# Kernel optimization log

Hardware: AMD Instinct MI355X
Metric: run time of the kernel (lower is better)

## Reference

```python
import jax, jax.numpy as jnp
import numpy as np

B, T, CIN, HID, OUT, H, W = 8, 8, 128, 64, 64, 32, 32


def _conv(x, w, b):
    # x: [B, C, H, W], w: [O, C, kh, kw] -> SAME-padded conv, stride 1
    y = jax.lax.conv_general_dilated(x, w, (1, 1), "SAME",
                                     dimension_numbers=("NCHW", "OIHW", "NCHW"))
    return y + b[None, :, None, None]


def _layer_dir(xs, w_ih, w_hh, b_ih, b_hh, reverse):
    # xs: [T, B, C, H, W]; one direction of a ConvLSTM layer; returns hs [T, B, HID, H, W]
    b, hh_, ww_ = xs.shape[1], xs.shape[3], xs.shape[4]
    h0 = jnp.zeros((b, HID, hh_, ww_), xs.dtype)

    def step(carry, x):
        h, c = carry
        gates = _conv(x, w_ih, b_ih) + _conv(h, w_hh, b_hh)  # [B, 4*HID, H, W]
        i, f, g, o = jnp.split(gates, 4, axis=1)
        c = jax.nn.sigmoid(f) * c + jax.nn.sigmoid(i) * jnp.tanh(g)
        h = jax.nn.sigmoid(o) * jnp.tanh(c)
        return (h, c), h

    _, hs = jax.lax.scan(step, (h0, h0), xs, reverse=reverse)
    return hs


def _forward(features, w_ih0f, w_hh0f, b_ih0f, b_hh0f,
             w_ih0r, w_hh0r, b_ih0r, b_hh0r,
             w_ih1f, w_hh1f, b_ih1f, b_hh1f,
             w_ih1r, w_hh1r, b_ih1r, b_hh1r,
             w_out, b_out):
    xs = jnp.transpose(features, (1, 0, 2, 3, 4))  # [T, B, C, H, W]
    # layer 0, both directions (scan reverse=True aligns outputs to original time order)
    hf = _layer_dir(xs, w_ih0f, w_hh0f, b_ih0f, b_hh0f, False)
    hr = _layer_dir(xs, w_ih0r, w_hh0r, b_ih0r, b_hh0r, True)
    xs1 = jnp.concatenate([hf, hr], axis=2)  # [T, B, 2*HID, H, W] (dropout is identity at eval)
    # layer 1
    hf1 = _layer_dir(xs1, w_ih1f, w_hh1f, b_ih1f, b_hh1f, False)
    hr1 = _layer_dir(xs1, w_ih1r, w_hh1r, b_ih1r, b_hh1r, True)
    last = jnp.concatenate([hf1[-1], hr1[-1]], axis=1)  # output[:, -1] -> [B, 2*HID, H, W]
    return jax.nn.relu(_conv(last, w_out, b_out))


def setup_inputs() -> dict:
    key = jax.random.key(0)
    ks = jax.random.split(key, 24)
    G = 4 * HID
    p = lambda k, s: jax.random.normal(k, s, jnp.float32) * 0.05
    d = {"features": jax.random.normal(ks[0], (B, T, CIN, H, W), jnp.float32)}
    i = 1
    for l, cin in ((0, CIN), (1, 2 * HID)):
        for dr in ("f", "r"):
            d[f"w_ih{l}{dr}"] = p(ks[i], (G, cin, 3, 3)); i += 1
            d[f"w_hh{l}{dr}"] = p(ks[i], (G, HID, 3, 3)); i += 1
            d[f"b_ih{l}{dr}"] = p(ks[i], (G,)); i += 1
            d[f"b_hh{l}{dr}"] = p(ks[i], (G,)); i += 1
    d["w_out"] = p(ks[i], (OUT, 2 * HID, 1, 1)); i += 1
    d["b_out"] = p(ks[i], (OUT,))
    return d


def reference(features, w_ih0f, w_hh0f, b_ih0f, b_hh0f,
              w_ih0r, w_hh0r, b_ih0r, b_hh0r,
              w_ih1f, w_hh1f, b_ih1f, b_hh1f,
              w_ih1r, w_hh1r, b_ih1r, b_hh1r,
              w_out, b_out):
    return _forward(features, w_ih0f, w_hh0f, b_ih0f, b_hh0f,
                    w_ih0r, w_hh0r, b_ih0r, b_hh0r,
                    w_ih1f, w_hh1f, b_ih1f, b_hh1f,
                    w_ih1r, w_hh1r, b_ih1r, b_hh1r,
                    w_out, b_out)
```

## Files before the change

kernel.cpp:

```cpp
#include <hip/hip_runtime.h>
#include <math.h>
#include <stdint.h>


typedef __attribute__((ext_vector_type(8))) short short8;
typedef __attribute__((ext_vector_type(4))) float float4v;

namespace {
constexpr int IMG = 34 * 34 * 64;
constexpr size_t SLOTI = 16ull * IMG;
constexpr int ROWB = 34 * 128;
constexpr int PADB = 8192;
}
template <int N> struct IC { static constexpr int v = N; };

__device__ __forceinline__ uint16_t bf16_rne(float x) {
  uint32_t u = __builtin_bit_cast(uint32_t, x);
  return (uint16_t)((u + 0x7FFFu + ((u >> 16) & 1u)) >> 16);
}
__device__ __forceinline__ float bf16_to_f(uint16_t h) {
  uint32_t u = ((uint32_t)h) << 16;
  return __builtin_bit_cast(float, u);
}

__device__ __forceinline__ void gl_lds16(const void* g, void* l) {
  __builtin_amdgcn_global_load_lds(
      (const __attribute__((address_space(1))) void*)g,
      (__attribute__((address_space(3))) void*)l, 16, 0, 0);
}

__global__ void pack_features(const float* __restrict__ f, uint16_t* __restrict__ out) {
  const size_t i = (size_t)blockIdx.x * 256 + threadIdx.x;
  const int blk_s = (int)(i & 7);
  size_t pp = i >> 3;
  const int px = (int)(pp % 34); pp /= 34;
  const int yy = (int)(pp % 34); pp /= 34;
  const int cg = (int)(pp & 3);
  const int bt = (int)(pp >> 2);
  const int b = bt & 7, t = bt >> 3;
  const int blk = blk_s ^ (px & 7);
  const int pl = blk >> 2, kg = blk & 3;
  short8 sv;
  if (px == 0 || px == 33 || yy == 0 || yy == 33) {
    #pragma unroll
    for (int j = 0; j < 8; ++j) sv[j] = 0;
  } else {
    const int x = px - 1, y = yy - 1;
    #pragma unroll
    for (int j = 0; j < 8; ++j) {
      const int ch = cg * 32 + kg * 8 + j;
      const float fv = f[(((size_t)b * 8 + t) * 128 + ch) * 1024 + y * 32 + x];
      const uint16_t hi = bf16_rne(fv);
      sv[j] = (short)(pl ? bf16_rne(fv - bf16_to_f(hi)) : hi);
    }
  }
  *(short8*)(out + i * 8) = sv;
}

struct WPackArgs {
  const float* wih[4]; const float* whh[4];
  const float* bih[4]; const float* bhh[4];
  uint32_t* wp; float* bp;
};
__global__ void pack_weights(WPackArgs A) {
  const int combo = blockIdx.y;
  const int idx = blockIdx.x * 256 + threadIdx.x;
  const int q = idx & 4095;
  const int rest = idx >> 12;
  const int nt = rest & 1;
  const int ct = rest >> 1;
  const int tap = ct % 9, cg = ct / 9;
  const int w2 = q & 3;
  const int b8s = (q >> 2) & 7;
  const int hcp = (q >> 5) & 15;
  const int g = (q >> 9) & 3;
  const int pl = (q >> 11) & 1;
  const int b8 = b8s ^ (hcp & 7);
  const int kg = b8 & 3;
  const int hcl = hcp * 2 + (b8 >> 2);
  const int n = g * 64 + nt * 32 + hcl;
  const float* wih = A.wih[combo];
  const float* whh = A.whh[combo];
  uint32_t out = 0;
  #pragma unroll
  for (int e = 0; e < 2; ++e) {
    const int ch = cg * 32 + kg * 8 + w2 * 2 + e;
    const float wv = (ch < 128) ? wih[((size_t)n * 128 + ch) * 9 + tap]
                                : whh[((size_t)n * 64 + (ch - 128)) * 9 + tap];
    const uint16_t hi = bf16_rne(wv);
    const uint16_t v = pl ? bf16_rne(wv - bf16_to_f(hi)) : hi;
    out |= ((uint32_t)v) << (16 * e);
  }
  A.wp[(size_t)combo * 442368 + idx] = out;
  if (idx < 256) A.bp[combo * 256 + idx] = A.bih[combo][idx] + A.bhh[combo][idx];
}

struct StepArgs {
  const uint16_t* in0; const uint16_t* in1; const uint16_t* in2;
  int nc0, nc1, nc2;
  const uint32_t* W;
  const float* bias;
  float* cbuf;
  uint16_t* himg;
  float* hf32;
};

template <int ROWS>
__global__ __launch_bounds__(ROWS * 128, ROWS / 2) void conv_lstm_step(StepArgs A0, StepArgs A1) {
  constexpr int NW = ROWS * 2;
  constexpr int THREADS = NW * 64;
  constexpr int BANDS = 32 / ROWS;
  constexpr int LOGB = (ROWS == 4) ? 3 : 4;
  constexpr int ACH = (ROWS == 4) ? 4 : 5;
  constexpr int ASLOT = ACH * NW * 1024;
  constexpr int WCH = 16384 / (NW * 1024);
  constexpr int CNT0 = WCH;
  constexpr int CNT12 = WCH + ACH;

  extern __shared__ char smem[];
  char* Asm_ = smem;
  char* Wsm_ = smem + 2 * ASLOT;

  const StepArgs a = (blockIdx.z == 0) ? A0 : A1;
  const int bx = blockIdx.x;
  const int nt = bx & 1;
  const int band = (bx >> 1) & (BANDS - 1);
  const int b = bx >> (1 + LOGB);
  const int y0 = band * ROWS;
  const int tid = threadIdx.x;
  const int lane = tid & 63;
  const int w = tid >> 6;
  const int m15 = lane & 15;
  const int kg = lane >> 4;
  const int r = w & (ROWS - 1);
  const int hcg = (ROWS == 4) ? (w >> 2) : (w >> 1);

  int offA[2][3][2];
  #pragma unroll
  for (int xh = 0; xh < 2; ++xh)
    #pragma unroll
    for (int kx = 0; kx < 3; ++kx)
      #pragma unroll
      for (int pl = 0; pl < 2; ++pl) {
        const int px = xh * 16 + kx + m15;
        const int sw = (pl * 4 + kg) ^ (px & 7);
        offA[xh][kx][pl] = r * ROWB + px * 128 + sw * 16;
      }
  int offW[2][4];
  {
    const int hcp = hcg * 8 + (m15 >> 1);
    const int b8 = kg + 4 * (m15 & 1);
    #pragma unroll
    for (int pl = 0; pl < 2; ++pl)
      #pragma unroll
      for (int g = 0; g < 4; ++g)
        offW[pl][g] = (((pl * 4 + g) * 16 + hcp) * 8 + (b8 ^ (hcp & 7))) * 16;
  }

  const int ncg = a.nc0 + a.nc1 + a.nc2;
  auto abase = [&](int cg) -> const char* {
    const uint16_t* t;
    if (cg < a.nc0) t = a.in0 + ((size_t)b * a.nc0 + cg) * IMG;
    else if (cg < a.nc0 + a.nc1) t = a.in1 + ((size_t)b * a.nc1 + (cg - a.nc0)) * IMG;
    else t = a.in2 + ((size_t)b * a.nc2 + (cg - a.nc0 - a.nc1)) * IMG;
    return (const char*)t + (size_t)y0 * ROWB;
  };
  auto stageA = [&](int cgi, int par) {
    const char* g = abase(cgi);
    char* d = Asm_ + par * ASLOT;
    #pragma unroll
    for (int j = 0; j < ACH; ++j)
      gl_lds16(g + (size_t)(ACH * w + j) * 1024 + lane * 16, d + (ACH * w + j) * 1024);
  };
  auto stageW = [&](int cgs, int taps, int slot) {
    const char* g = (const char*)a.W + ((size_t)((cgs * 9 + taps) * 2 + nt) << 14);
    char* d = Wsm_ + slot * 16384;
    #pragma unroll
    for (int j = 0; j < WCH; ++j)
      gl_lds16(g + (size_t)(WCH * w + j) * 1024 + lane * 16, d + (WCH * w + j) * 1024);
  };

  float4v acc[2][4];
  #pragma unroll
  for (int xh = 0; xh < 2; ++xh)
    #pragma unroll
    for (int g = 0; g < 4; ++g) acc[xh][g] = (float4v){0.f, 0.f, 0.f, 0.f};

  stageA(0, 0);
  stageW(0, 0, 0);
  stageW(0, 1, 1);

  for (int cg = 0; cg < ncg; ++cg) {
    auto tap_body = [&](auto tapc) {
      constexpr int TAP = decltype(tapc)::v;
      constexpr int CNT = (TAP == 1 || TAP == 2) ? CNT12 : CNT0;
      asm volatile("s_waitcnt vmcnt(%0)\n\ts_barrier" :: "n"(CNT) : "memory");
      const int lin = cg * 9 + TAP;
      {
        const int l2 = lin + 2;
        int cgs = l2 / 9;
        const int taps = l2 % 9;
        if (cgs >= ncg) cgs = 0;
        stageW(cgs, taps, l2 % 3);
      }
      if (TAP == 0) {
        const int nx = (cg + 1 < ncg) ? cg + 1 : 0;
        stageA(nx, (cg + 1) & 1);
      }
      constexpr int ky = TAP / 3, kx = TAP % 3;
      const char* Ab = Asm_ + (cg & 1) * ASLOT + ky * ROWB;
      const char* Wb = Wsm_ + (lin % 3) * 16384;
      short8 af[2][2];
      #pragma unroll
      for (int xh = 0; xh < 2; ++xh)
        #pragma unroll
        for (int pl = 0; pl < 2; ++pl)
          af[xh][pl] = *(const short8*)(Ab + offA[xh][kx][pl]);
      short8 wfr[2][4];
      #pragma unroll
      for (int pl = 0; pl < 2; ++pl)
        #pragma unroll
        for (int g = 0; g < 4; ++g)
          wfr[pl][g] = *(const short8*)(Wb + offW[pl][g]);
      #pragma unroll
      for (int xh = 0; xh < 2; ++xh)
        #pragma unroll
        for (int g = 0; g < 4; ++g) {
          acc[xh][g] = __builtin_amdgcn_mfma_f32_16x16x32_bf16(af[xh][0], wfr[0][g], acc[xh][g], 0, 0, 0);
          acc[xh][g] = __builtin_amdgcn_mfma_f32_16x16x32_bf16(af[xh][0], wfr[1][g], acc[xh][g], 0, 0, 0);
          acc[xh][g] = __builtin_amdgcn_mfma_f32_16x16x32_bf16(af[xh][1], wfr[0][g], acc[xh][g], 0, 0, 0);
        }
    };
    tap_body(IC<0>{}); tap_body(IC<1>{}); tap_body(IC<2>{});
    tap_body(IC<3>{}); tap_body(IC<4>{}); tap_body(IC<5>{});
    tap_body(IC<6>{}); tap_body(IC<7>{}); tap_body(IC<8>{});
  }
  asm volatile("s_waitcnt vmcnt(0)" ::: "memory");

  const int hcl = hcg * 16 + m15;
  const int hc = nt * 32 + hcl;
  const int y = y0 + r;
  float bi[4];
  #pragma unroll
  for (int g = 0; g < 4; ++g) bi[g] = a.bias[g * 64 + hc];
  float* crow = a.cbuf + ((size_t)(b * 64 + hc)) * 1024 + y * 32;
  float* hrow = a.hf32 ? a.hf32 + ((size_t)(b * 64 + hc)) * 1024 + y * 32 : nullptr;
  uint16_t* hb = a.himg ? a.himg + ((size_t)(b * 2 + nt)) * IMG : nullptr;
  const int kgb = hcl >> 3, jj = hcl & 7;
  #pragma unroll
  for (int xh = 0; xh < 2; ++xh) {
    const int x0 = xh * 16 + kg * 4;
    float4v cv = *(float4v*)(crow + x0);
    float4v cn, hn;
    #pragma unroll
    for (int q = 0; q < 4; ++q) {
      const float ig = 1.f / (1.f + expf(-(acc[xh][0][q] + bi[0])));
      const float fg = 1.f / (1.f + expf(-(acc[xh][1][q] + bi[1])));
      const float gg = tanhf(acc[xh][2][q] + bi[2]);
      const float og = 1.f / (1.f + expf(-(acc[xh][3][q] + bi[3])));
      const float c2 = fg * cv[q] + ig * gg;
      cn[q] = c2;
      hn[q] = og * tanhf(c2);
    }
    *(float4v*)(crow + x0) = cn;
    if (hrow) *(float4v*)(hrow + x0) = hn;
    if (hb) {
      #pragma unroll
      for (int q = 0; q < 4; ++q) {
        const int px = x0 + q + 1;
        const int sw = px & 7;
        const uint16_t hi = bf16_rne(hn[q]);
        const uint16_t lo = bf16_rne(hn[q] - bf16_to_f(hi));
        const size_t p16 = ((size_t)(y + 1) * 34 + px) * 64;
        hb[p16 + (size_t)(kgb ^ sw) * 8 + jj] = hi;
        hb[p16 + (size_t)((4 + kgb) ^ sw) * 8 + jj] = lo;
      }
    }
  }
  if (hb) {
    {
      const int rr = tid >> 7;
      const int hlf = (tid >> 6) & 1;
      const int jx = tid & 63;
      hb[((size_t)(y0 + 1 + rr) * 34 + hlf * 33) * 64 + jx] = 0;
    }
    if (band == 0) for (int i = tid; i < 2176; i += THREADS) hb[i] = 0;
    if (band == BANDS - 1) for (int i = tid; i < 2176; i += THREADS) hb[(size_t)33 * 2176 + i] = 0;
  }
}

__global__ void final_conv(const float* __restrict__ h1f_last, const float* __restrict__ h1r_last,
                           const float* __restrict__ wout, const float* __restrict__ bout,
                           float* __restrict__ out) {
  __shared__ float Ws[16 * 128];
  const int oq = blockIdx.y;
  for (int i = threadIdx.x; i < 16 * 128; i += 256) Ws[i] = wout[oq * 16 * 128 + i];
  __syncthreads();
  const int gp = blockIdx.x * 256 + threadIdx.x;
  const int b = gp >> 10, p = gp & 1023;
  float acc[16];
  #pragma unroll
  for (int o = 0; o < 16; ++o) acc[o] = bout[oq * 16 + o];
  for (int c = 0; c < 128; ++c) {
    const float xv = (c < 64) ? h1f_last[((size_t)b * 64 + c) * 1024 + p]
                              : h1r_last[((size_t)b * 64 + (c - 64)) * 1024 + p];
    #pragma unroll
    for (int o = 0; o < 16; ++o) acc[o] = fmaf(xv, Ws[o * 128 + c], acc[o]);
  }
  #pragma unroll
  for (int o = 0; o < 16; ++o) {
    const float v = acc[o];
    out[((size_t)b * 64 + oq * 16 + o) * 1024 + p] = v > 0.f ? v : 0.f;
  }
}

extern "C" void kernel_launch(void* const* d_in, const int* in_sizes, int n_in,
                              void* d_out, int out_size, void* d_ws, size_t ws_size,
                              hipStream_t stream) {
  char* p = (char*)d_ws;
  uint16_t* featImg = (uint16_t*)p; p += (size_t)8 * 8 * 4 * IMG * 2 + PADB;
  uint32_t* WP = (uint32_t*)p;      p += (size_t)4 * 442368 * 4;
  float* bp = (float*)p;            p += 4096;
  uint16_t* hf0i = (uint16_t*)p;    p += (size_t)9 * SLOTI * 2 + PADB;
  uint16_t* hr0i = (uint16_t*)p;    p += (size_t)9 * SLOTI * 2 + PADB;
  uint16_t* h1fi = (uint16_t*)p;    p += (size_t)2 * SLOTI * 2 + PADB;
  float* c0f = (float*)p;           p += (size_t)4 * 2097152;
  float* c0r = c0f + 524288;
  float* c1f = c0r + 524288;
  float* c1r = c1f + 524288;
  float* h1f8 = (float*)p;          p += 2097152;
  float* h1r8 = (float*)p;          p += 2097152;

  hipMemsetAsync(c0f, 0, (size_t)4 * 2097152, stream);
  hipMemsetAsync(hf0i, 0, (size_t)SLOTI * 2, stream);
  hipMemsetAsync(hr0i + (size_t)8 * SLOTI, 0, (size_t)SLOTI * 2, stream);
  hipMemsetAsync(h1fi, 0, (size_t)SLOTI * 2, stream);

  pack_features<<<dim3(9248), 256, 0, stream>>>((const float*)d_in[0], featImg);

  WPackArgs wa;
  for (int combo = 0; combo < 4; ++combo) {
    const int base = 1 + combo * 4;
    wa.wih[combo] = (const float*)d_in[base];
    wa.whh[combo] = (const float*)d_in[base + 1];
    wa.bih[combo] = (const float*)d_in[base + 2];
    wa.bhh[combo] = (const float*)d_in[base + 3];
  }
  wa.wp = WP; wa.bp = bp;
  pack_weights<<<dim3(1728, 4), 256, 0, stream>>>(wa);

  constexpr int DYN4 = 2 * 32768 + 3 * 16384;
  constexpr int DYN2 = 2 * 20480 + 3 * 16384;
  (void)hipFuncSetAttribute((const void*)(conv_lstm_step<4>),
                            hipFuncAttributeMaxDynamicSharedMemorySize, DYN4);
  (void)hipFuncSetAttribute((const void*)(conv_lstm_step<2>),
                            hipFuncAttributeMaxDynamicSharedMemorySize, DYN2);

  auto mk = [&](const uint16_t* i0, int n0, const uint16_t* i1, int n1,
                const uint16_t* i2, int n2, int combo, float* cb,
                uint16_t* himg, float* hf32) {
    StepArgs s;
    s.in0 = i0; s.in1 = i1; s.in2 = i2;
    s.nc0 = n0; s.nc1 = n1; s.nc2 = n2;
    s.W = WP + (size_t)combo * 442368; s.bias = bp + combo * 256;
    s.cbuf = cb; s.himg = himg; s.hf32 = hf32;
    return s;
  };

  for (int k = 0; k < 8; ++k) {
    const int tr = 7 - k;
    StepArgs f = mk(featImg + (size_t)k * 8 * 4 * IMG, 4,
                    hf0i + (size_t)k * SLOTI, 2, nullptr, 0,
                    0, c0f, hf0i + (size_t)(k + 1) * SLOTI, nullptr);
    StepArgs r = mk(featImg + (size_t)tr * 8 * 4 * IMG, 4,
                    hr0i + (size_t)(tr + 1) * SLOTI, 2, nullptr, 0,
                    1, c0r, hr0i + (size_t)tr * SLOTI, nullptr);
    conv_lstm_step<4><<<dim3(128, 1, 2), 512, DYN4, stream>>>(f, r);
  }

  for (int t = 0; t < 8; ++t) {
    uint16_t* himg = (t < 7) ? h1fi + (size_t)((t + 1) & 1) * SLOTI : nullptr;
    float* hf32 = (t == 7) ? h1f8 : nullptr;
    StepArgs s = mk(hf0i + (size_t)(t + 1) * SLOTI, 2, hr0i + (size_t)t * SLOTI, 2,
                    h1fi + (size_t)(t & 1) * SLOTI, 2, 2, c1f, himg, hf32);
    if (t == 0) {
      StepArgs rv = mk(hf0i + (size_t)8 * SLOTI, 2, hr0i + (size_t)7 * SLOTI, 2,
                       nullptr, 0, 3, c1r, nullptr, h1r8);
      conv_lstm_step<4><<<dim3(128, 1, 2), 512, DYN4, stream>>>(s, rv);
    } else {
      conv_lstm_step<2><<<dim3(256, 1, 1), 256, DYN2, stream>>>(s, s);
    }
  }

  final_conv<<<dim3(32, 4), 256, 0, stream>>>(
      h1f8, h1r8, (const float*)d_in[17], (const float*)d_in[18], (float*)d_out);
}
```

Before: 725.5 us.

## Retile ConvLSTM step blocks to 16 channels and two rows per wave

Each block now covers 16 hidden channels (a quarter of the gate outputs) across more image rows, and every wave computes two output rows, so each weight fragment loaded from LDS feeds twice as many MFMAs. Weight staging per block is halved to 8KB per tap, while the input halo tile grows. Blocks have fewer waves (4 or 2) and launch bounds are relaxed to 1, which doubles accumulator registers per wave and lowers the wave count per block, so latency hiding may suffer.

```diff
diff --git a/kernel.cpp b/kernel.cpp
--- a/kernel.cpp
+++ b/kernel.cpp
@@ -105,15 +105,15 @@
   float* hf32;
 };
 
-template <int ROWS>
-__global__ __launch_bounds__(ROWS * 128, ROWS / 2) void conv_lstm_step(StepArgs A0, StepArgs A1) {
-  constexpr int NW = ROWS * 2;
+template <int ROWS, int NW>
+__global__ __launch_bounds__(NW * 64, 1) void conv_lstm_step(StepArgs A0, StepArgs A1) {
   constexpr int THREADS = NW * 64;
   constexpr int BANDS = 32 / ROWS;
-  constexpr int LOGB = (ROWS == 4) ? 3 : 4;
-  constexpr int ACH = (ROWS == 4) ? 4 : 5;
+  constexpr int BSH = (ROWS == 8) ? 2 : 3;
+  constexpr int ABYTES = (ROWS + 2) * ROWB;
+  constexpr int ACH = (ABYTES + NW * 1024 - 1) / (NW * 1024);
   constexpr int ASLOT = ACH * NW * 1024;
-  constexpr int WCH = 16384 / (NW * 1024);
+  constexpr int WCH = 8 / NW;
   constexpr int CNT0 = WCH;
   constexpr int CNT12 = WCH + ACH;
 
@@ -123,38 +123,40 @@
 
   const StepArgs a = (blockIdx.z == 0) ? A0 : A1;
   const int bx = blockIdx.x;
-  const int nt = bx & 1;
-  const int band = (bx >> 1) & (BANDS - 1);
-  const int b = bx >> (1 + LOGB);
+  const int Q4 = bx & 3;
+  const int band = (bx >> 2) & (BANDS - 1);
+  const int b = bx >> (2 + BSH);
+  const int nt = Q4 >> 1;
+  const int nq = Q4 & 1;
   const int y0 = band * ROWS;
   const int tid = threadIdx.x;
   const int lane = tid & 63;
   const int w = tid >> 6;
   const int m15 = lane & 15;
   const int kg = lane >> 4;
-  const int r = w & (ROWS - 1);
-  const int hcg = (ROWS == 4) ? (w >> 2) : (w >> 1);
-
-  int offA[2][3][2];
-  #pragma unroll
-  for (int xh = 0; xh < 2; ++xh)
-    #pragma unroll
-    for (int kx = 0; kx < 3; ++kx)
-      #pragma unroll
-      for (int pl = 0; pl < 2; ++pl) {
-        const int px = xh * 16 + kx + m15;
-        const int sw = (pl * 4 + kg) ^ (px & 7);
-        offA[xh][kx][pl] = r * ROWB + px * 128 + sw * 16;
-      }
+
+  int offA[2][2][3][2];
+  #pragma unroll
+  for (int row = 0; row < 2; ++row)
+    #pragma unroll
+    for (int xh = 0; xh < 2; ++xh)
+      #pragma unroll
+      for (int kx = 0; kx < 3; ++kx)
+        #pragma unroll
+        for (int pl = 0; pl < 2; ++pl) {
+          const int px = xh * 16 + kx + m15;
+          const int sw = (pl * 4 + kg) ^ (px & 7);
+          offA[row][xh][kx][pl] = (2 * w + row) * ROWB + px * 128 + sw * 16;
+        }
   int offW[2][4];
   {
-    const int hcp = hcg * 8 + (m15 >> 1);
+    const int hcpl = m15 >> 1;
     const int b8 = kg + 4 * (m15 & 1);
     #pragma unroll
     for (int pl = 0; pl < 2; ++pl)
       #pragma unroll
       for (int g = 0; g < 4; ++g)
-        offW[pl][g] = (((pl * 4 + g) * 16 + hcp) * 8 + (b8 ^ (hcp & 7))) * 16;
+        offW[pl][g] = (((pl * 4 + g) * 8 + hcpl) * 8 + (b8 ^ hcpl)) * 16;
   }
 
   const int ncg = a.nc0 + a.nc1 + a.nc2;
@@ -173,18 +175,23 @@
       gl_lds16(g + (size_t)(ACH * w + j) * 1024 + lane * 16, d + (ACH * w + j) * 1024);
   };
   auto stageW = [&](int cgs, int taps, int slot) {
-    const char* g = (const char*)a.W + ((size_t)((cgs * 9 + taps) * 2 + nt) << 14);
-    char* d = Wsm_ + slot * 16384;
-    #pragma unroll
-    for (int j = 0; j < WCH; ++j)
-      gl_lds16(g + (size_t)(WCH * w + j) * 1024 + lane * 16, d + (WCH * w + j) * 1024);
+    const char* g = (const char*)a.W + ((size_t)((cgs * 9 + taps) * 2 + nt) << 14)
+                  + (size_t)nq * 1024;
+    char* d = Wsm_ + slot * 8192;
+    #pragma unroll
+    for (int j = 0; j < WCH; ++j) {
+      const int c = WCH * w + j;
+      gl_lds16(g + (size_t)c * 2048 + lane * 16, d + c * 1024);
+    }
   };
 
-  float4v acc[2][4];
-  #pragma unroll
-  for (int xh = 0; xh < 2; ++xh)
-    #pragma unroll
-    for (int g = 0; g < 4; ++g) acc[xh][g] = (float4v){0.f, 0.f, 0.f, 0.f};
+  float4v acc[2][2][4];
+  #pragma unroll
+  for (int row = 0; row < 2; ++row)
+    #pragma unroll
+    for (int xh = 0; xh < 2; ++xh)
+      #pragma unroll
+      for (int g = 0; g < 4; ++g) acc[row][xh][g] = (float4v){0.f, 0.f, 0.f, 0.f};
 
   stageA(0, 0);
   stageW(0, 0, 0);
@@ -209,13 +216,15 @@
       }
       constexpr int ky = TAP / 3, kx = TAP % 3;
       const char* Ab = Asm_ + (cg & 1) * ASLOT + ky * ROWB;
-      const char* Wb = Wsm_ + (lin % 3) * 16384;
-      short8 af[2][2];
-      #pragma unroll
-      for (int xh = 0; xh < 2; ++xh)
+      const char* Wb = Wsm_ + (lin % 3) * 8192;
+      short8 af[2][2][2];
+      #pragma unroll
+      for (int row = 0; row < 2; ++row)
         #pragma unroll
-        for (int pl = 0; pl < 2; ++pl)
-          af[xh][pl] = *(const short8*)(Ab + offA[xh][kx][pl]);
+        for (int xh = 0; xh < 2; ++xh)
+          #pragma unroll
+          for (int pl = 0; pl < 2; ++pl)
+            af[row][xh][pl] = *(const short8*)(Ab + offA[row][xh][kx][pl]);
       short8 wfr[2][4];
       #pragma unroll
       for (int pl = 0; pl < 2; ++pl)
@@ -223,13 +232,15 @@
         for (int g = 0; g < 4; ++g)
           wfr[pl][g] = *(const short8*)(Wb + offW[pl][g]);
       #pragma unroll
-      for (int xh = 0; xh < 2; ++xh)
+      for (int row = 0; row < 2; ++row)
         #pragma unroll
-        for (int g = 0; g < 4; ++g) {
-          acc[xh][g] = __builtin_amdgcn_mfma_f32_16x16x32_bf16(af[xh][0], wfr[0][g], acc[xh][g], 0, 0, 0);
-          acc[xh][g] = __builtin_amdgcn_mfma_f32_16x16x32_bf16(af[xh][0], wfr[1][g], acc[xh][g], 0, 0, 0);
-          acc[xh][g] = __builtin_amdgcn_mfma_f32_16x16x32_bf16(af[xh][1], wfr[0][g], acc[xh][g], 0, 0, 0);
-        }
+        for (int xh = 0; xh < 2; ++xh)
+          #pragma unroll
+          for (int g = 0; g < 4; ++g) {
+            acc[row][xh][g] = __builtin_amdgcn_mfma_f32_16x16x32_bf16(af[row][xh][0], wfr[0][g], acc[row][xh][g], 0, 0, 0);
+            acc[row][xh][g] = __builtin_amdgcn_mfma_f32_16x16x32_bf16(af[row][xh][0], wfr[1][g], acc[row][xh][g], 0, 0, 0);
+            acc[row][xh][g] = __builtin_amdgcn_mfma_f32_16x16x32_bf16(af[row][xh][1], wfr[0][g], acc[row][xh][g], 0, 0, 0);
+          }
     };
     tap_body(IC<0>{}); tap_body(IC<1>{}); tap_body(IC<2>{});
     tap_body(IC<3>{}); tap_body(IC<4>{}); tap_body(IC<5>{});
@@ -237,51 +248,55 @@
   }
   asm volatile("s_waitcnt vmcnt(0)" ::: "memory");
 
-  const int hcl = hcg * 16 + m15;
-  const int hc = nt * 32 + hcl;
-  const int y = y0 + r;
+  const int hc = Q4 * 16 + m15;
   float bi[4];
   #pragma unroll
   for (int g = 0; g < 4; ++g) bi[g] = a.bias[g * 64 + hc];
-  float* crow = a.cbuf + ((size_t)(b * 64 + hc)) * 1024 + y * 32;
-  float* hrow = a.hf32 ? a.hf32 + ((size_t)(b * 64 + hc)) * 1024 + y * 32 : nullptr;
-  uint16_t* hb = a.himg ? a.himg + ((size_t)(b * 2 + nt)) * IMG : nullptr;
-  const int kgb = hcl >> 3, jj = hcl & 7;
-  #pragma unroll
-  for (int xh = 0; xh < 2; ++xh) {
-    const int x0 = xh * 16 + kg * 4;
-    float4v cv = *(float4v*)(crow + x0);
-    float4v cn, hn;
-    #pragma unroll
-    for (int q = 0; q < 4; ++q) {
-      const float ig = 1.f / (1.f + expf(-(acc[xh][0][q] + bi[0])));
-      const float fg = 1.f / (1.f + expf(-(acc[xh][1][q] + bi[1])));
-      const float gg = tanhf(acc[xh][2][q] + bi[2]);
-      const float og = 1.f / (1.f + expf(-(acc[xh][3][q] + bi[3])));
-      const float c2 = fg * cv[q] + ig * gg;
-      cn[q] = c2;
-      hn[q] = og * tanhf(c2);
-    }
-    *(float4v*)(crow + x0) = cn;
-    if (hrow) *(float4v*)(hrow + x0) = hn;
-    if (hb) {
+  const int img = Q4 >> 1;
+  const int chi = (Q4 & 1) * 16 + m15;
+  const int kgb = chi >> 3, jj = chi & 7;
+  uint16_t* hb = a.himg ? a.himg + ((size_t)(b * 2 + img)) * IMG : nullptr;
+  #pragma unroll
+  for (int row = 0; row < 2; ++row) {
+    const int y = y0 + 2 * w + row;
+    float* crow = a.cbuf + ((size_t)(b * 64 + hc)) * 1024 + y * 32;
+    float* hrow = a.hf32 ? a.hf32 + ((size_t)(b * 64 + hc)) * 1024 + y * 32 : nullptr;
+    #pragma unroll
+    for (int xh = 0; xh < 2; ++xh) {
+      const int x0 = xh * 16 + kg * 4;
+      float4v cv = *(float4v*)(crow + x0);
+      float4v cn, hn;
       #pragma unroll
       for (int q = 0; q < 4; ++q) {
-        const int px = x0 + q + 1;
-        const int sw = px & 7;
-        const uint16_t hi = bf16_rne(hn[q]);
-        const uint16_t lo = bf16_rne(hn[q] - bf16_to_f(hi));
-        const size_t p16 = ((size_t)(y + 1) * 34 + px) * 64;
-        hb[p16 + (size_t)(kgb ^ sw) * 8 + jj] = hi;
-        hb[p16 + (size_t)((4 + kgb) ^ sw) * 8 + jj] = lo;
+        const float ig = 1.f / (1.f + expf(-(acc[row][xh][0][q] + bi[0])));
+        const float fg = 1.f / (1.f + expf(-(acc[row][xh][1][q] + bi[1])));
+        const float gg = tanhf(acc[row][xh][2][q] + bi[2]);
+        const float og = 1.f / (1.f + expf(-(acc[row][xh][3][q] + bi[3])));
+        const float c2 = fg * cv[q] + ig * gg;
+        cn[q] = c2;
+        hn[q] = og * tanhf(c2);
+      }
+      *(float4v*)(crow + x0) = cn;
+      if (hrow) *(float4v*)(hrow + x0) = hn;
+      if (hb) {
+        #pragma unroll
+        for (int q = 0; q < 4; ++q) {
+          const int px = x0 + q + 1;
+          const int sw = px & 7;
+          const uint16_t hi = bf16_rne(hn[q]);
+          const uint16_t lo = bf16_rne(hn[q] - bf16_to_f(hi));
+          const size_t p16 = ((size_t)(y + 1) * 34 + px) * 64;
+          hb[p16 + (size_t)(kgb ^ sw) * 8 + jj] = hi;
+          hb[p16 + (size_t)((4 + kgb) ^ sw) * 8 + jj] = lo;
+        }
       }
     }
   }
   if (hb) {
-    {
-      const int rr = tid >> 7;
-      const int hlf = (tid >> 6) & 1;
-      const int jx = tid & 63;
+    for (int i = tid; i < ROWS * 128; i += THREADS) {
+      const int rr = i >> 7;
+      const int hlf = (i >> 6) & 1;
+      const int jx = i & 63;
       hb[((size_t)(y0 + 1 + rr) * 34 + hlf * 33) * 64 + jx] = 0;
     }
     if (band == 0) for (int i = tid; i < 2176; i += THREADS) hb[i] = 0;
@@ -349,12 +364,12 @@
   wa.wp = WP; wa.bp = bp;
   pack_weights<<<dim3(1728, 4), 256, 0, stream>>>(wa);
 
-  constexpr int DYN4 = 2 * 32768 + 3 * 16384;
-  constexpr int DYN2 = 2 * 20480 + 3 * 16384;
-  (void)hipFuncSetAttribute((const void*)(conv_lstm_step<4>),
-                            hipFuncAttributeMaxDynamicSharedMemorySize, DYN4);
-  (void)hipFuncSetAttribute((const void*)(conv_lstm_step<2>),
-                            hipFuncAttributeMaxDynamicSharedMemorySize, DYN2);
+  constexpr int DYN_P = 2 * 45056 + 3 * 8192;
+  constexpr int DYN_S = 2 * 26624 + 3 * 8192;
+  (void)hipFuncSetAttribute((const void*)(conv_lstm_step<8, 4>),
+                            hipFuncAttributeMaxDynamicSharedMemorySize, DYN_P);
+  (void)hipFuncSetAttribute((const void*)(conv_lstm_step<4, 2>),
+                            hipFuncAttributeMaxDynamicSharedMemorySize, DYN_S);
 
   auto mk = [&](const uint16_t* i0, int n0, const uint16_t* i1, int n1,
                 const uint16_t* i2, int n2, int combo, float* cb,
@@ -375,7 +390,7 @@
     StepArgs r = mk(featImg + (size_t)tr * 8 * 4 * IMG, 4,
                     hr0i + (size_t)(tr + 1) * SLOTI, 2, nullptr, 0,
                     1, c0r, hr0i + (size_t)tr * SLOTI, nullptr);
-    conv_lstm_step<4><<<dim3(128, 1, 2), 512, DYN4, stream>>>(f, r);
+    conv_lstm_step<8, 4><<<dim3(128, 1, 2), 256, DYN_P, stream>>>(f, r);
   }
 
   for (int t = 0; t < 8; ++t) {
@@ -386,9 +401,9 @@
     if (t == 0) {
       StepArgs rv = mk(hf0i + (size_t)8 * SLOTI, 2, hr0i + (size_t)7 * SLOTI, 2,
                        nullptr, 0, 3, c1r, nullptr, h1r8);
-      conv_lstm_step<4><<<dim3(128, 1, 2), 512, DYN4, stream>>>(s, rv);
+      conv_lstm_step<8, 4><<<dim3(128, 1, 2), 256, DYN_P, stream>>>(s, rv);
     } else {
-      conv_lstm_step<2><<<dim3(256, 1, 1), 256, DYN2, stream>>>(s, s);
+      conv_lstm_step<4, 2><<<dim3(256, 1, 1), 128, DYN_S, stream>>>(s, s);
     }
   }
 
```

After: 811.6 us. 11.9% more time.
